# Kernel optimization log

Hardware: AMD Instinct MI355X
Metric: run time of the kernel (lower is better)

The kernel has to match this reference:

```python
import jax, jax.numpy as jnp
from jax import lax
import numpy as np

B, T, I, H, L, C = 64, 512, 256, 1024, 2, 2


def setup_inputs() -> dict:
    key = jax.random.key(0)
    ks = jax.random.split(key, 11)
    s_in = 1.0 / np.sqrt(H)
    return {
        "x": jax.random.normal(ks[0], (B, T, I), jnp.float32),
        "W_ih0": jax.random.normal(ks[1], (4 * H, I), jnp.float32) * s_in,
        "W_hh0": jax.random.normal(ks[2], (4 * H, H), jnp.float32) * s_in,
        "b_ih0": jax.random.normal(ks[3], (4 * H,), jnp.float32) * s_in,
        "b_hh0": jax.random.normal(ks[4], (4 * H,), jnp.float32) * s_in,
        "W_ih1": jax.random.normal(ks[5], (4 * H, H), jnp.float32) * s_in,
        "W_hh1": jax.random.normal(ks[6], (4 * H, H), jnp.float32) * s_in,
        "b_ih1": jax.random.normal(ks[7], (4 * H,), jnp.float32) * s_in,
        "b_hh1": jax.random.normal(ks[8], (4 * H,), jnp.float32) * s_in,
        "fc_w": jax.random.normal(ks[9], (C, H), jnp.float32) * s_in,
        "fc_b": jax.random.normal(ks[10], (C,), jnp.float32) * s_in,
    }


def _lstm_layer(x, W_ih, W_hh, b_ih, b_hh):
    # x: [B, T, in]; PyTorch gate order: i, f, g, o
    b, t = x.shape[0], x.shape[1]
    h0 = jnp.zeros((b, H), x.dtype)
    c0 = jnp.zeros((b, H), x.dtype)
    # precompute all input projections in one big GEMM: [B, T, 4H]
    xp = jnp.einsum('bti,gi->btg', x, W_ih) + b_ih + b_hh

    def step(carry, xt):
        h, c = carry
        g = xt + h @ W_hh.T  # [B, 4H]
        i_g, f_g, g_g, o_g = jnp.split(g, 4, axis=-1)
        i_g = jax.nn.sigmoid(i_g)
        f_g = jax.nn.sigmoid(f_g)
        g_g = jnp.tanh(g_g)
        o_g = jax.nn.sigmoid(o_g)
        c = f_g * c + i_g * g_g
        h = o_g * jnp.tanh(c)
        return (h, c), h

    (hT, cT), hs = lax.scan(step, (h0, c0), xp.transpose(1, 0, 2))
    return hs.transpose(1, 0, 2), hT  # [B, T, H], [B, H]


def reference(x, W_ih0, W_hh0, b_ih0, b_hh0, W_ih1, W_hh1, b_ih1, b_hh1, fc_w, fc_b):
    y0, h0T = _lstm_layer(x, W_ih0, W_hh0, b_ih0, b_hh0)
    _, h1T = _lstm_layer(y0, W_ih1, W_hh1, b_ih1, b_hh1)
    # hn: [num_layers, B, H] -> view(-1, H) -> [L*B, H]
    hn = jnp.concatenate([h0T, h1T], axis=0)  # [2B, H]
    out = jax.nn.relu(hn)
    out = out @ fc_w.T + fc_b  # [2B, C]
    return jax.nn.sigmoid(out)
```

## Files before the change

### kernel.cpp

```cpp
#include <hip/hip_runtime.h>
#include <hip/hip_bf16.h>
#include <hip/hip_fp16.h>
#include <stdint.h>

#define BB 64
#define TT 512
#define II 256
#define HH 1024
#define G4 4096

typedef unsigned short u16;
typedef unsigned long long u64;
typedef __attribute__((ext_vector_type(8))) _Float16 h8;
typedef __attribute__((ext_vector_type(4))) float f32x4;

__device__ __forceinline__ u16 f2h(float x){
  _Float16 h = (_Float16)x;
  return __builtin_bit_cast(u16, h);
}
__device__ __forceinline__ float sigm(float x){ return 1.0f/(1.0f + __expf(-x)); }
__device__ __forceinline__ float tanh_f(float x){ return 1.0f - 2.0f/(1.0f + __expf(2.0f*x)); }

__device__ __forceinline__ void cld16(h8& dst, const u16* p){
  asm volatile("global_load_dwordx4 %0, %1, off sc0 sc1" : "=v"(dst) : "v"(p));
}
__device__ __forceinline__ void vm_drain(){
  asm volatile("s_waitcnt vmcnt(0)" ::: "memory");
  __builtin_amdgcn_sched_barrier(0);
}

__global__ void bias_comb_kernel(const float* __restrict__ a, const float* __restrict__ b,
                                 float* __restrict__ o, int n){
  int i = blockIdx.x*blockDim.x + threadIdx.x;
  if (i < n) o[i] = a[i] + b[i];
}

__global__ void xconv_kernel(const float* __restrict__ x, u16* __restrict__ xb){
  int m = blockIdx.x;
  int t = m >> 6, b = m & 63;
  const float4* src = (const float4*)(x + ((size_t)b*TT + t)*II);
  float4 v = src[threadIdx.x];
  ushort4 o; o.x=f2h(v.x); o.y=f2h(v.y); o.z=f2h(v.z); o.w=f2h(v.w);
  ((ushort4*)(xb + (size_t)m*II))[threadIdx.x] = o;
}

__global__ void wswz_kernel(const float* __restrict__ Wa, int Ka,
                            const float* __restrict__ Wb, int Kb,
                            u16* __restrict__ dst, int KS){
  int s8 = blockIdx.x*blockDim.x + threadIdx.x;
  int lane = s8 & 63;
  int f    = (s8 >> 6) & 1;
  int rest = s8 >> 7;
  int ks   = rest % KS;
  int jg8  = rest / KS;
  if (jg8 >= 128) return;
  int id = lane & 15, quad = lane >> 4;
  int g = f*2 + (id >> 3);
  int n = g*HH + jg8*8 + (id & 7);
  int k = ks*32 + quad*8;
  const float* src = (k < Ka) ? (Wa + (size_t)n*Ka + k) : (Wb + (size_t)n*Kb + (k - Ka));
  float4 v0 = ((const float4*)src)[0];
  float4 v1 = ((const float4*)src)[1];
  ushort4 o0; o0.x=f2h(v0.x); o0.y=f2h(v0.y); o0.z=f2h(v0.z); o0.w=f2h(v0.w);
  ushort4 o1; o1.x=f2h(v1.x); o1.y=f2h(v1.y); o1.z=f2h(v1.z); o1.w=f2h(v1.w);
  u16* d = dst + (size_t)s8*8;
  ((ushort4*)d)[0] = o0;
  ((ushort4*)d)[1] = o1;
}

__launch_bounds__(256, 1)
__global__ void lstm_fused_kernel(const u16* __restrict__ xb,
                                  const u16* __restrict__ Wsw0,
                                  const u16* __restrict__ Wsw1,
                                  const float* __restrict__ bias0,
                                  const float* __restrict__ bias1,
                                  u16* __restrict__ h0buf,
                                  u16* __restrict__ h1buf,
                                  float* __restrict__ hfin,
                                  int* __restrict__ stamp0,
                                  int* __restrict__ stamp1){
  __shared__ float Gs[4][32][68];
  const int blk = blockIdx.x;
  const int layer = blk >> 7;
  const int jg = blk & 127;
  const int tid = threadIdx.x, wave = tid >> 6, lane = tid & 63;
  const int id = lane & 15, quad = lane >> 4;
  const int KS = layer ? 64 : 40;
  const u16* Wblk = (layer ? Wsw1 : Wsw0) + (size_t)jg * KS * 1024;
  const int cb = tid >> 2, jq = tid & 3;
  const int j0 = jg * 8;
  const float* Bp = layer ? bias1 : bias0;
  float bs[4][2];
  #pragma unroll
  for (int g = 0; g < 4; ++g)
    #pragma unroll
    for (int jj = 0; jj < 2; ++jj)
      bs[g][jj] = Bp[g*HH + j0 + jq*2 + jj];
  float c2[2] = {0.f, 0.f};

  if (layer == 0){
    h8 w0[10], w1[10];
    #pragma unroll
    for (int i = 0; i < 10; ++i){
      int ks = (i < 2) ? (2*wave + i) : (8 + 8*wave + (i - 2));
      const u16* wl = Wblk + (size_t)ks*1024 + lane*8;
      w0[i] = *(const h8*)(wl);
      w1[i] = *(const h8*)(wl + 512);
    }
    const int* myst = stamp0 + (wave*32 + (lane & 31))*32;
    int credit = 0;
    for (int t = 0; t < TT; ++t){
      const u16* hA = h0buf + ((size_t)(t & 7) << 16);
      u16* hout     = h0buf + ((size_t)((t + 1) & 7) << 16);
      f32x4 a0[4] = {}, a1[4] = {};
      #pragma unroll
      for (int i = 0; i < 2; ++i){
        int xcol = (2*wave + i)*32 + quad*8;
        #pragma unroll
        for (int mt = 0; mt < 4; ++mt){
          h8 A = *(const h8*)(xb + (((size_t)t*64 + mt*16 + id) << 8) + xcol);
          a0[mt] = __builtin_amdgcn_mfma_f32_16x16x32_f16(A, w0[i], a0[mt], 0,0,0);
          a1[mt] = __builtin_amdgcn_mfma_f32_16x16x32_f16(A, w1[i], a1[mt], 0,0,0);
        }
      }
      while (__hip_atomic_load(myst, __ATOMIC_RELAXED, __HIP_MEMORY_SCOPE_AGENT) < t)
        __builtin_amdgcn_s_sleep(2);
      if (wave == 0){
        while (credit < t - 7){
          int sa = __hip_atomic_load(stamp1 + lane*32,      __ATOMIC_RELAXED, __HIP_MEMORY_SCOPE_AGENT);
          int sb = __hip_atomic_load(stamp1 + (64+lane)*32, __ATOMIC_RELAXED, __HIP_MEMORY_SCOPE_AGENT);
          int s = sa < sb ? sa : sb;
          #pragma unroll
          for (int off = 32; off; off >>= 1){
            int s2 = __shfl_xor(s, off);
            s = s < s2 ? s : s2;
          }
          credit = s;
          if (credit < t - 7) __builtin_amdgcn_s_sleep(8);
        }
      }
      {
        h8 st[32];
        #pragma unroll
        for (int i = 0; i < 8; ++i){
          int hcol = wave*256 + i*32 + quad*8;
          #pragma unroll
          for (int mt = 0; mt < 4; ++mt)
            cld16(st[i*4 + mt], hA + ((size_t)(mt*16 + id) << 10) + hcol);
        }
        vm_drain();
        #pragma unroll
        for (int i = 0; i < 8; ++i)
          #pragma unroll
          for (int mt = 0; mt < 4; ++mt){
            a0[mt] = __builtin_amdgcn_mfma_f32_16x16x32_f16(st[i*4+mt], w0[2+i], a0[mt], 0,0,0);
            a1[mt] = __builtin_amdgcn_mfma_f32_16x16x32_f16(st[i*4+mt], w1[2+i], a1[mt], 0,0,0);
          }
      }
      #pragma unroll
      for (int mt = 0; mt < 4; ++mt){
        *(f32x4*)&Gs[wave][id][mt*16 + quad*4]      = a0[mt];
        *(f32x4*)&Gs[wave][16 + id][mt*16 + quad*4] = a1[mt];
      }
      __syncthreads();
      ushort2 hb; float2 hf;
      #pragma unroll
      for (int jj = 0; jj < 2; ++jj){
        int jl = jq*2 + jj;
        float p[4];
        #pragma unroll
        for (int g = 0; g < 4; ++g){
          int e = (g >> 1)*16 + (g & 1)*8 + jl;
          p[g] = Gs[0][e][cb] + Gs[1][e][cb] + Gs[2][e][cb] + Gs[3][e][cb] + bs[g][jj];
        }
        float iv = sigm(p[0]), fv = sigm(p[1]), gv = tanh_f(p[2]), ov = sigm(p[3]);
        float c = fv*c2[jj] + iv*gv;
        c2[jj] = c;
        float h = ov * tanh_f(c);
        (&hf.x)[jj] = h;
        ((u16*)&hb)[jj] = f2h(h);
      }
      union { ushort2 s; unsigned int v; } pk; pk.s = hb;
      __hip_atomic_store((unsigned int*)&hout[(size_t)cb*HH + j0 + jq*2],
                         pk.v, __ATOMIC_RELAXED, __HIP_MEMORY_SCOPE_AGENT);
      if (t == TT - 1)
        *(float2*)&hfin[(size_t)cb*HH + j0 + jq*2] = hf;
      __syncthreads();
      if (tid == 0)
        __hip_atomic_store(stamp0 + jg*32, t + 1, __ATOMIC_RELAXED, __HIP_MEMORY_SCOPE_AGENT);
    }
  } else {
    h8 w0[16], w1[16];
    const int wb = wave * 16;
    #pragma unroll
    for (int l = 0; l < 16; ++l){
      const u16* wl = Wblk + (size_t)(wb + l)*1024 + lane*8;
      w0[l] = *(const h8*)(wl);
      w1[l] = *(const h8*)(wl + 512);
    }
    const int koff = (wave & 1) * 512;
    const int* myst = ((wave < 2) ? stamp0 : stamp1) + ((wave & 1)*64 + lane)*32;
    for (int t = 0; t < TT; ++t){
      const u16* y0  = h0buf + ((size_t)((t + 1) & 7) << 16);
      const u16* hA1 = h1buf + ((size_t)(t & 7) << 16);
      u16* hout      = h1buf + ((size_t)((t + 1) & 7) << 16);
      const u16* hsrc = (wave < 2) ? y0 : hA1;
      const int need  = (wave < 2) ? (t + 1) : t;
      while (__hip_atomic_load(myst, __ATOMIC_RELAXED, __HIP_MEMORY_SCOPE_AGENT) < need)
        __builtin_amdgcn_s_sleep(2);
      f32x4 a0[4] = {}, a1[4] = {};
      {
        h8 st[32];
        #pragma unroll
        for (int l = 0; l < 8; ++l){
          int col = koff + l*32 + quad*8;
          #pragma unroll
          for (int mt = 0; mt < 4; ++mt)
            cld16(st[l*4 + mt], hsrc + ((size_t)(mt*16 + id) << 10) + col);
        }
        vm_drain();
        #pragma unroll
        for (int l = 0; l < 8; ++l)
          #pragma unroll
          for (int mt = 0; mt < 4; ++mt){
            a0[mt] = __builtin_amdgcn_mfma_f32_16x16x32_f16(st[l*4+mt], w0[l], a0[mt], 0,0,0);
            a1[mt] = __builtin_amdgcn_mfma_f32_16x16x32_f16(st[l*4+mt], w1[l], a1[mt], 0,0,0);
          }
      }
      {
        h8 st[32];
        #pragma unroll
        for (int l = 0; l < 8; ++l){
          int col = koff + (8 + l)*32 + quad*8;
          #pragma unroll
          for (int mt = 0; mt < 4; ++mt)
            cld16(st[l*4 + mt], hsrc + ((size_t)(mt*16 + id) << 10) + col);
        }
        vm_drain();
        #pragma unroll
        for (int l = 0; l < 8; ++l)
          #pragma unroll
          for (int mt = 0; mt < 4; ++mt){
            a0[mt] = __builtin_amdgcn_mfma_f32_16x16x32_f16(st[l*4+mt], w0[8+l], a0[mt], 0,0,0);
            a1[mt] = __builtin_amdgcn_mfma_f32_16x16x32_f16(st[l*4+mt], w1[8+l], a1[mt], 0,0,0);
          }
      }
      #pragma unroll
      for (int mt = 0; mt < 4; ++mt){
        *(f32x4*)&Gs[wave][id][mt*16 + quad*4]      = a0[mt];
        *(f32x4*)&Gs[wave][16 + id][mt*16 + quad*4] = a1[mt];
      }
      __syncthreads();
      ushort2 hb; float2 hf;
      #pragma unroll
      for (int jj = 0; jj < 2; ++jj){
        int jl = jq*2 + jj;
        float p[4];
        #pragma unroll
        for (int g = 0; g < 4; ++g){
          int e = (g >> 1)*16 + (g & 1)*8 + jl;
          p[g] = Gs[0][e][cb] + Gs[1][e][cb] + Gs[2][e][cb] + Gs[3][e][cb] + bs[g][jj];
        }
        float iv = sigm(p[0]), fv = sigm(p[1]), gv = tanh_f(p[2]), ov = sigm(p[3]);
        float c = fv*c2[jj] + iv*gv;
        c2[jj] = c;
        float h = ov * tanh_f(c);
        (&hf.x)[jj] = h;
        ((u16*)&hb)[jj] = f2h(h);
      }
      union { ushort2 s; unsigned int v; } pk; pk.s = hb;
      __hip_atomic_store((unsigned int*)&hout[(size_t)cb*HH + j0 + jq*2],
                         pk.v, __ATOMIC_RELAXED, __HIP_MEMORY_SCOPE_AGENT);
      if (t == TT - 1)
        *(float2*)&hfin[(size_t)(BB*HH) + (size_t)cb*HH + j0 + jq*2] = hf;
      __syncthreads();
      if (tid == 0)
        __hip_atomic_store(stamp1 + jg*32, t + 1, __ATOMIC_RELAXED, __HIP_MEMORY_SCOPE_AGENT);
    }
  }
}

__global__ void fc_kernel(const float* __restrict__ hfin, const float* __restrict__ fcw,
                          const float* __restrict__ fcb, float* __restrict__ out){
  int row = blockIdx.x;
  int lane = threadIdx.x;
  const float* h = hfin + (size_t)row*HH;
  float a0 = 0.f, a1 = 0.f;
  for (int j = lane; j < HH; j += 64){
    float v = h[j]; v = v > 0.f ? v : 0.f;
    a0 += v * fcw[j];
    a1 += v * fcw[HH + j];
  }
  for (int off = 32; off; off >>= 1){ a0 += __shfl_down(a0, off); a1 += __shfl_down(a1, off); }
  if (lane == 0){
    out[row*2 + 0] = 1.f/(1.f + __expf(-(a0 + fcb[0])));
    out[row*2 + 1] = 1.f/(1.f + __expf(-(a1 + fcb[1])));
  }
}

extern "C" void kernel_launch(void* const* d_in, const int* in_sizes, int n_in,
                              void* d_out, int out_size, void* d_ws, size_t ws_size,
                              hipStream_t stream){
  (void)in_sizes; (void)n_in; (void)out_size; (void)ws_size;
  const float* x    = (const float*)d_in[0];
  const float* Wih0 = (const float*)d_in[1];
  const float* Whh0 = (const float*)d_in[2];
  const float* bih0 = (const float*)d_in[3];
  const float* bhh0 = (const float*)d_in[4];
  const float* Wih1 = (const float*)d_in[5];
  const float* Whh1 = (const float*)d_in[6];
  const float* bih1 = (const float*)d_in[7];
  const float* bhh1 = (const float*)d_in[8];
  const float* fcw  = (const float*)d_in[9];
  const float* fcb  = (const float*)d_in[10];

  char* w = (char*)d_ws;
  size_t off = 0;
  auto take = [&](size_t bytes)->char*{
    char* p = w + off; off += (bytes + 255) & ~(size_t)255; return p;
  };
  u16*   xb    = (u16*)  take((size_t)TT*BB*II*2);
  u16*   wsw0  = (u16*)  take((size_t)G4*1280*2);
  u16*   wsw1  = (u16*)  take((size_t)G4*2048*2);
  float* bias0 = (float*)take(G4*4);
  float* bias1 = (float*)take(G4*4);
  u16*   h0buf = (u16*)  take(8*(size_t)BB*HH*2);
  u16*   h1buf = (u16*)  take(8*(size_t)BB*HH*2);
  float* hfin  = (float*)take(2*(size_t)BB*HH*4);
  int*   stamp0= (int*)  take(128*128);
  int*   stamp1= (int*)  take(128*128);

  hipMemsetAsync(h0buf, 0, 8*(size_t)BB*HH*2, stream);
  hipMemsetAsync(h1buf, 0, 8*(size_t)BB*HH*2, stream);
  hipMemsetAsync(stamp0, 0, 128*128, stream);
  hipMemsetAsync(stamp1, 0, 128*128, stream);

  bias_comb_kernel<<<16, 256, 0, stream>>>(bih0, bhh0, bias0, G4);
  bias_comb_kernel<<<16, 256, 0, stream>>>(bih1, bhh1, bias1, G4);
  xconv_kernel<<<TT*BB, 64, 0, stream>>>(x, xb);
  wswz_kernel<<<2560, 256, 0, stream>>>(Wih0, II, Whh0, HH, wsw0, 40);
  wswz_kernel<<<4096, 256, 0, stream>>>(Wih1, HH, Whh1, HH, wsw1, 64);

  lstm_fused_kernel<<<256, 256, 0, stream>>>(xb, wsw0, wsw1, bias0, bias1,
                                             h0buf, h1buf, hfin, stamp0, stamp1);
  fc_kernel<<<2*BB, 64, 0, stream>>>(hfin, fcw, fcb, (float*)d_out);
}
```

Baseline: 5.056 ms.

## Replace per-step stamp polling with sentinel-tagged hidden-state buffers

Removes the stamp0 flag wait. Consumers instead load hidden state directly and retry whenever any fp16 element still holds an infinity sentinel. Producers clear a slot eight steps ahead, and the ring grows from 8 to 16 slots to make room. The aim is to drop a serialized flag round-trip and one barrier from each recurrent step, at the cost of possible repeated full loads while spinning. It also relies on the sentinel value never occurring as a real hidden value and on store ordering within each 16-byte load.

Result: slower. 6.595 ms (+30.4%).

```diff
diff --git a/kernel.cpp b/kernel.cpp
--- a/kernel.cpp
+++ b/kernel.cpp
@@ -8,6 +8,7 @@
 #define II 256
 #define HH 1024
 #define G4 4096
+#define SENT 0x7C00u
 
 typedef unsigned short u16;
 typedef unsigned long long u64;
@@ -28,11 +29,48 @@
   asm volatile("s_waitcnt vmcnt(0)" ::: "memory");
   __builtin_amdgcn_sched_barrier(0);
 }
+__device__ __forceinline__ bool stale16(h8 v){
+  union { h8 h; unsigned d[4]; } u; u.h = v;
+  bool b = false;
+  #pragma unroll
+  for (int k = 0; k < 4; ++k) b |= ((u.d[k] & 0xFFFFu) == SENT);
+  return b;
+}
+
+#define LOADV32(STARR, SRC, COLBASE) do {                                        \
+  for(;;){                                                                       \
+    _Pragma("unroll")                                                            \
+    for (int i_ = 0; i_ < 8; ++i_){                                              \
+      int col_ = (COLBASE) + i_*32 + quad*8;                                     \
+      _Pragma("unroll")                                                          \
+      for (int mt_ = 0; mt_ < 4; ++mt_)                                          \
+        cld16(STARR[i_*4 + mt_], (SRC) + ((size_t)(mt_*16 + id) << 10) + col_);  \
+    }                                                                            \
+    vm_drain();                                                                  \
+    bool bad_ = false;                                                           \
+    _Pragma("unroll")                                                            \
+    for (int i_ = 0; i_ < 32; ++i_) bad_ |= stale16(STARR[i_]);                  \
+    if (!__any(bad_)) break;                                                     \
+    __builtin_amdgcn_s_sleep(1);                                                 \
+  }                                                                              \
+} while(0)
+
+__device__ __forceinline__ void end_barrier(){
+  asm volatile("s_waitcnt lgkmcnt(0)\n\ts_barrier" ::: "memory");
+}
 
 __global__ void bias_comb_kernel(const float* __restrict__ a, const float* __restrict__ b,
                                  float* __restrict__ o, int n){
   int i = blockIdx.x*blockDim.x + threadIdx.x;
   if (i < n) o[i] = a[i] + b[i];
+}
+
+__global__ void hinit_kernel(unsigned* __restrict__ h0, unsigned* __restrict__ h1){
+  int i = blockIdx.x*blockDim.x + threadIdx.x;
+  unsigned slot = ((unsigned)i) >> 15;
+  unsigned v = (slot == 0) ? 0u : (SENT | (SENT << 16));
+  h0[i] = v;
+  h1[i] = v;
 }
 
 __global__ void xconv_kernel(const float* __restrict__ x, u16* __restrict__ xb){
@@ -77,7 +115,6 @@
                                   u16* __restrict__ h0buf,
                                   u16* __restrict__ h1buf,
                                   float* __restrict__ hfin,
-                                  int* __restrict__ stamp0,
                                   int* __restrict__ stamp1){
   __shared__ float Gs[4][32][68];
   const int blk = blockIdx.x;
@@ -107,11 +144,11 @@
       w0[i] = *(const h8*)(wl);
       w1[i] = *(const h8*)(wl + 512);
     }
-    const int* myst = stamp0 + (wave*32 + (lane & 31))*32;
     int credit = 0;
     for (int t = 0; t < TT; ++t){
-      const u16* hA = h0buf + ((size_t)(t & 7) << 16);
-      u16* hout     = h0buf + ((size_t)((t + 1) & 7) << 16);
+      const u16* hA = h0buf + ((size_t)(t & 15) << 16);
+      u16* hout     = h0buf + ((size_t)((t + 1) & 15) << 16);
+      u16* hrst     = h0buf + ((size_t)((t + 9) & 15) << 16);
       f32x4 a0[4] = {}, a1[4] = {};
       #pragma unroll
       for (int i = 0; i < 2; ++i){
@@ -123,8 +160,6 @@
           a1[mt] = __builtin_amdgcn_mfma_f32_16x16x32_f16(A, w1[i], a1[mt], 0,0,0);
         }
       }
-      while (__hip_atomic_load(myst, __ATOMIC_RELAXED, __HIP_MEMORY_SCOPE_AGENT) < t)
-        __builtin_amdgcn_s_sleep(2);
       if (wave == 0){
         while (credit < t - 7){
           int sa = __hip_atomic_load(stamp1 + lane*32,      __ATOMIC_RELAXED, __HIP_MEMORY_SCOPE_AGENT);
@@ -141,14 +176,7 @@
       }
       {
         h8 st[32];
-        #pragma unroll
-        for (int i = 0; i < 8; ++i){
-          int hcol = wave*256 + i*32 + quad*8;
-          #pragma unroll
-          for (int mt = 0; mt < 4; ++mt)
-            cld16(st[i*4 + mt], hA + ((size_t)(mt*16 + id) << 10) + hcol);
-        }
-        vm_drain();
+        LOADV32(st, hA, wave*256);
         #pragma unroll
         for (int i = 0; i < 8; ++i)
           #pragma unroll
@@ -183,11 +211,11 @@
       union { ushort2 s; unsigned int v; } pk; pk.s = hb;
       __hip_atomic_store((unsigned int*)&hout[(size_t)cb*HH + j0 + jq*2],
                          pk.v, __ATOMIC_RELAXED, __HIP_MEMORY_SCOPE_AGENT);
+      __hip_atomic_store((unsigned int*)&hrst[(size_t)cb*HH + j0 + jq*2],
+                         SENT | (SENT << 16), __ATOMIC_RELAXED, __HIP_MEMORY_SCOPE_AGENT);
       if (t == TT - 1)
         *(float2*)&hfin[(size_t)cb*HH + j0 + jq*2] = hf;
-      __syncthreads();
-      if (tid == 0)
-        __hip_atomic_store(stamp0 + jg*32, t + 1, __ATOMIC_RELAXED, __HIP_MEMORY_SCOPE_AGENT);
+      end_barrier();
     }
   } else {
     h8 w0[16], w1[16];
@@ -199,26 +227,16 @@
       w1[l] = *(const h8*)(wl + 512);
     }
     const int koff = (wave & 1) * 512;
-    const int* myst = ((wave < 2) ? stamp0 : stamp1) + ((wave & 1)*64 + lane)*32;
     for (int t = 0; t < TT; ++t){
-      const u16* y0  = h0buf + ((size_t)((t + 1) & 7) << 16);
-      const u16* hA1 = h1buf + ((size_t)(t & 7) << 16);
-      u16* hout      = h1buf + ((size_t)((t + 1) & 7) << 16);
+      const u16* y0  = h0buf + ((size_t)((t + 1) & 15) << 16);
+      const u16* hA1 = h1buf + ((size_t)(t & 15) << 16);
+      u16* hout      = h1buf + ((size_t)((t + 1) & 15) << 16);
+      u16* hrst      = h1buf + ((size_t)((t + 9) & 15) << 16);
       const u16* hsrc = (wave < 2) ? y0 : hA1;
-      const int need  = (wave < 2) ? (t + 1) : t;
-      while (__hip_atomic_load(myst, __ATOMIC_RELAXED, __HIP_MEMORY_SCOPE_AGENT) < need)
-        __builtin_amdgcn_s_sleep(2);
       f32x4 a0[4] = {}, a1[4] = {};
       {
         h8 st[32];
-        #pragma unroll
-        for (int l = 0; l < 8; ++l){
-          int col = koff + l*32 + quad*8;
-          #pragma unroll
-          for (int mt = 0; mt < 4; ++mt)
-            cld16(st[l*4 + mt], hsrc + ((size_t)(mt*16 + id) << 10) + col);
-        }
-        vm_drain();
+        LOADV32(st, hsrc, koff);
         #pragma unroll
         for (int l = 0; l < 8; ++l)
           #pragma unroll
@@ -229,14 +247,7 @@
       }
       {
         h8 st[32];
-        #pragma unroll
-        for (int l = 0; l < 8; ++l){
-          int col = koff + (8 + l)*32 + quad*8;
-          #pragma unroll
-          for (int mt = 0; mt < 4; ++mt)
-            cld16(st[l*4 + mt], hsrc + ((size_t)(mt*16 + id) << 10) + col);
-        }
-        vm_drain();
+        LOADV32(st, hsrc, koff + 256);
         #pragma unroll
         for (int l = 0; l < 8; ++l)
           #pragma unroll
@@ -271,9 +282,11 @@
       union { ushort2 s; unsigned int v; } pk; pk.s = hb;
       __hip_atomic_store((unsigned int*)&hout[(size_t)cb*HH + j0 + jq*2],
                          pk.v, __ATOMIC_RELAXED, __HIP_MEMORY_SCOPE_AGENT);
+      __hip_atomic_store((unsigned int*)&hrst[(size_t)cb*HH + j0 + jq*2],
+                         SENT | (SENT << 16), __ATOMIC_RELAXED, __HIP_MEMORY_SCOPE_AGENT);
       if (t == TT - 1)
         *(float2*)&hfin[(size_t)(BB*HH) + (size_t)cb*HH + j0 + jq*2] = hf;
-      __syncthreads();
+      end_barrier();
       if (tid == 0)
         __hip_atomic_store(stamp1 + jg*32, t + 1, __ATOMIC_RELAXED, __HIP_MEMORY_SCOPE_AGENT);
     }
@@ -324,24 +337,21 @@
   u16*   wsw1  = (u16*)  take((size_t)G4*2048*2);
   float* bias0 = (float*)take(G4*4);
   float* bias1 = (float*)take(G4*4);
-  u16*   h0buf = (u16*)  take(8*(size_t)BB*HH*2);
-  u16*   h1buf = (u16*)  take(8*(size_t)BB*HH*2);
+  u16*   h0buf = (u16*)  take(16*(size_t)BB*HH*2);
+  u16*   h1buf = (u16*)  take(16*(size_t)BB*HH*2);
   float* hfin  = (float*)take(2*(size_t)BB*HH*4);
-  int*   stamp0= (int*)  take(128*128);
   int*   stamp1= (int*)  take(128*128);
 
-  hipMemsetAsync(h0buf, 0, 8*(size_t)BB*HH*2, stream);
-  hipMemsetAsync(h1buf, 0, 8*(size_t)BB*HH*2, stream);
-  hipMemsetAsync(stamp0, 0, 128*128, stream);
   hipMemsetAsync(stamp1, 0, 128*128, stream);
 
   bias_comb_kernel<<<16, 256, 0, stream>>>(bih0, bhh0, bias0, G4);
   bias_comb_kernel<<<16, 256, 0, stream>>>(bih1, bhh1, bias1, G4);
+  hinit_kernel<<<2048, 256, 0, stream>>>((unsigned*)h0buf, (unsigned*)h1buf);
   xconv_kernel<<<TT*BB, 64, 0, stream>>>(x, xb);
   wswz_kernel<<<2560, 256, 0, stream>>>(Wih0, II, Whh0, HH, wsw0, 40);
   wswz_kernel<<<4096, 256, 0, stream>>>(Wih1, HH, Whh1, HH, wsw1, 64);
 
   lstm_fused_kernel<<<256, 256, 0, stream>>>(xb, wsw0, wsw1, bias0, bias1,
-                                             h0buf, h1buf, hfin, stamp0, stamp1);
+                                             h0buf, h1buf, hfin, stamp1);
   fc_kernel<<<2*BB, 64, 0, stream>>>(hfin, fcw, fcb, (float*)d_out);
 }
```
